# Kernel optimization log

Hardware: AMD Instinct MI355X
Metric: run time of the kernel (lower is better)

The kernel has to match this reference:

```python
import jax, jax.numpy as jnp
import numpy as np

N, E, D = 20000, 320000, 128


def _glorot(key, shape):
    fan_in, fan_out = shape[0], shape[-1]
    lim = jnp.sqrt(6.0 / (fan_in + fan_out)).astype(jnp.float32)
    return jax.random.uniform(key, shape, jnp.float32, -lim, lim)


def setup_inputs() -> dict:
    key = jax.random.key(0)
    ks = jax.random.split(key, 16)
    h = jax.random.normal(ks[0], (N, 1, D), jnp.float32)
    x = jax.random.normal(ks[1], (N, 3), jnp.float32)
    edge_index = jax.random.randint(ks[2], (2, E), 0, N, jnp.int64)
    # edge_mlp: SPDMLP(2D -> D -> D), 2 linear layers with ReLU between
    W1e = _glorot(ks[3], (2 * D, D)); b1e = jnp.zeros((D,), jnp.float32)
    W2e = _glorot(ks[4], (D, D));     b2e = jnp.zeros((D,), jnp.float32)
    # edge_inf: Linear(D, 1) + Sigmoid
    Wg = _glorot(ks[5], (D, 1));      bg = jnp.zeros((1,), jnp.float32)
    # node_mlp: SPDMLP(2D -> D -> D)
    W1n = _glorot(ks[6], (2 * D, D)); b1n = jnp.zeros((D,), jnp.float32)
    W2n = _glorot(ks[7], (D, D));     b2n = jnp.zeros((D,), jnp.float32)
    return {"h": h, "x": x, "edge_index": edge_index,
            "W1e": W1e, "b1e": b1e, "W2e": W2e, "b2e": b2e,
            "Wg": Wg, "bg": bg,
            "W1n": W1n, "b1n": b1n, "W2n": W2n, "b2n": b2n}


def _feature_joint(a, b):
    # a: [B, Na, Da], b: [B, Nb, Db] -> [B, Na+Nb, Da+Db] block-diagonal concat
    Da, Db = a.shape[2], b.shape[2]
    a_exp = jnp.concatenate([a, jnp.zeros(a.shape[:2] + (Db,), a.dtype)], axis=2)
    b_exp = jnp.concatenate([jnp.zeros(b.shape[:2] + (Da,), b.dtype), b], axis=2)
    return jnp.concatenate([a_exp, b_exp], axis=1)


def _mlp2(y, W1, b1, W2, b2):
    return jax.nn.relu(y @ W1 + b1) @ W2 + b2


def reference(h, x, edge_index, W1e, b1e, W2e, b2e, Wg, bg, W1n, b1n, W2n, b2n):
    src, dst = edge_index[0], edge_index[1]
    hi, hj = h[dst], h[src]                              # [E, 1, D] each
    mij = _mlp2(_feature_joint(hi, hj), W1e, b1e, W2e, b2e)  # [E, 2, D]
    eij = jax.nn.sigmoid(mij @ Wg + bg)                  # [E, 2, 1]
    mi = jax.ops.segment_sum(mij * eij, dst, num_segments=h.shape[0])  # [N, 2, D]
    h_new = h + _mlp2(_feature_joint(mi, h), W1n, b1n, W2n, b2n)       # [N, 3, D]
    return (h_new, x)
```

## Files before the change

### kernel.cpp

```cpp
#include <hip/hip_runtime.h>

#define D   128
#define SP  136
#define FS  132
#define NC  2
#define CAP 64

typedef __attribute__((ext_vector_type(8))) short bf16x8;
typedef __attribute__((ext_vector_type(4))) float f32x4;
typedef unsigned short u16;

__device__ __forceinline__ float sigmoidf(float v) { return 1.0f / (1.0f + __expf(-v)); }

__device__ __forceinline__ u16 f2bf(float x) {
    union { float f; unsigned u; } c; c.f = x;
    return (u16)((c.u + 0x7fffu + ((c.u >> 16) & 1u)) >> 16);
}
__device__ __forceinline__ float bflo(unsigned u) {
    union { unsigned v; float f; } c; c.v = u << 16; return c.f;
}
__device__ __forceinline__ float bfhi(unsigned u) {
    union { unsigned v; float f; } c; c.v = u & 0xffff0000u; return c.f;
}

__device__ __forceinline__ void layer_mfma(
    const u16* __restrict__ a_hi,
    const short* __restrict__ WbM, int lane, int ctbase, f32x4 acc[NC][2])
{
    #pragma unroll
    for (int ks = 0; ks < 4; ++ks) {
        bf16x8 ah[2];
        #pragma unroll
        for (int rt = 0; rt < 2; ++rt) {
            const int o = (rt * 16 + (lane & 15)) * SP + ks * 32 + (lane >> 4) * 8;
            ah[rt] = *reinterpret_cast<const bf16x8*>(a_hi + o);
        }
        #pragma unroll
        for (int c = 0; c < NC; ++c) {
            const bf16x8 bh = *reinterpret_cast<const bf16x8*>(
                WbM + ((ctbase + c) * 4 + ks) * 512 + lane * 8);
            #pragma unroll
            for (int rt = 0; rt < 2; ++rt)
                acc[c][rt] = __builtin_amdgcn_mfma_f32_16x16x32_bf16(ah[rt], bh, acc[c][rt], 0, 0, 0);
        }
    }
}

__device__ __forceinline__ void store_relu(
    const f32x4 acc[NC][2], const float b1v[NC],
    u16* __restrict__ t_hi, int lane, int ctbase)
{
    #pragma unroll
    for (int c = 0; c < NC; ++c)
        #pragma unroll
        for (int rt = 0; rt < 2; ++rt)
            #pragma unroll
            for (int rr = 0; rr < 4; ++rr) {
                const int row = rt * 16 + (lane >> 4) * 4 + rr;
                const int j   = (ctbase + c) * 16 + (lane & 15);
                t_hi[row * SP + j] = f2bf(fmaxf(acc[c][rt][rr] + b1v[c], 0.f));
            }
}

__device__ __forceinline__ void acc8(float* a, uint4 q) {
    a[0] += bflo(q.x); a[1] += bfhi(q.x);
    a[2] += bflo(q.y); a[3] += bfhi(q.y);
    a[4] += bflo(q.z); a[5] += bfhi(q.z);
    a[6] += bflo(q.w); a[7] += bfhi(q.w);
}

__device__ __forceinline__ void mlp_core(
    int base, int r, int N,
    const float* __restrict__ h,  const float* __restrict__ R0,
    const int* __restrict__ cnt,  const int* __restrict__ bucket,
    const u16* __restrict__ Q1b,  const short* __restrict__ Wb,
    const float* __restrict__ b1n, const float* __restrict__ b2n,
    float* __restrict__ out_h, u16* __restrict__ smem)
{
    u16* a_hi = smem;
    u16* t_hi = smem + 32 * SP;

    const int tid  = threadIdx.x, lane = tid & 63, w = tid >> 6;
    const int ctbase = w * NC;
    const int nl = tid >> 3, cg = tid & 7;

    if (r == 1) {
        int node = base + nl; if (node >= N) node = N - 1;
        int deg = cnt[node]; if (deg > CAP) deg = CAP;
        const int* __restrict__ bk = bucket + (size_t)node * CAP;
        const u16* __restrict__ Qc = Q1b + cg * 16;
        float a[16] = {0.f,0.f,0.f,0.f,0.f,0.f,0.f,0.f,0.f,0.f,0.f,0.f,0.f,0.f,0.f,0.f};
        for (int i = 0; i < deg; ++i) {
            const int s = bk[i];
            const uint4 qa = *reinterpret_cast<const uint4*>(Qc + (size_t)s * D);
            const uint4 qb = *reinterpret_cast<const uint4*>(Qc + (size_t)s * D + 8);
            acc8(a, qa); acc8(a + 8, qb);
        }
        union { u16 s[16]; uint4 v[2]; } ph;
        #pragma unroll
        for (int k = 0; k < 16; ++k) ph.s[k] = f2bf(a[k]);
        *reinterpret_cast<uint4*>(&a_hi[nl * SP + cg * 16])     = ph.v[0];
        *reinterpret_cast<uint4*>(&a_hi[nl * SP + cg * 16 + 8]) = ph.v[1];
    } else {
        const float* __restrict__ src = (r == 0) ? R0 : h;
        for (int idx = tid; idx < 32 * 32; idx += 256) {
            const int row = idx >> 5, c4 = (idx & 31) << 2;
            int node = base + row; if (node >= N) node = N - 1;
            float4 v = *reinterpret_cast<const float4*>(&src[(size_t)node * D + c4]);
            if (r == 0) {
                const float cv = (float)cnt[node];
                v.x *= cv; v.y *= cv; v.z *= cv; v.w *= cv;
            }
            ushort4 hi;
            hi.x = f2bf(v.x); hi.y = f2bf(v.y); hi.z = f2bf(v.z); hi.w = f2bf(v.w);
            *reinterpret_cast<ushort4*>(&a_hi[row * SP + c4]) = hi;
        }
    }
    __syncthreads();

    float b1v[NC], b2v[NC];
    #pragma unroll
    for (int c = 0; c < NC; ++c) {
        const int j = (ctbase + c) * 16 + (lane & 15);
        b1v[c] = b1n[j]; b2v[c] = b2n[j];
    }

    f32x4 acc[NC][2];
    #pragma unroll
    for (int c = 0; c < NC; ++c)
        #pragma unroll
        for (int rt = 0; rt < 2; ++rt) acc[c][rt] = (f32x4){0.f, 0.f, 0.f, 0.f};
    layer_mfma(a_hi, Wb + (size_t)((r == 2) ? 4 : 3) * 16384, lane, ctbase, acc);
    __syncthreads();
    store_relu(acc, b1v, t_hi, lane, ctbase);
    __syncthreads();

    f32x4 o[NC][2];
    #pragma unroll
    for (int c = 0; c < NC; ++c)
        #pragma unroll
        for (int rt = 0; rt < 2; ++rt) o[c][rt] = (f32x4){0.f, 0.f, 0.f, 0.f};
    layer_mfma(t_hi, Wb + (size_t)5 * 16384, lane, ctbase, o);
    __syncthreads();

    float* fs = reinterpret_cast<float*>(smem);
    #pragma unroll
    for (int c = 0; c < NC; ++c)
        #pragma unroll
        for (int rt = 0; rt < 2; ++rt)
            #pragma unroll
            for (int rr = 0; rr < 4; ++rr) {
                const int row = rt * 16 + (lane >> 4) * 4 + rr;
                const int j   = (ctbase + c) * 16 + (lane & 15);
                fs[row * FS + j] = o[c][rt][rr] + b2v[c];
            }
    __syncthreads();

    const int node = base + nl;
    if (node < N) {
        #pragma unroll
        for (int k = 0; k < 4; ++k) {
            float4 ov = *reinterpret_cast<const float4*>(&fs[nl * FS + cg * 16 + k * 4]);
            const float4 hv = *reinterpret_cast<const float4*>(&h[(size_t)node * D + cg * 16 + k * 4]);
            ov.x += hv.x; ov.y += hv.y; ov.z += hv.z; ov.w += hv.w;
            *reinterpret_cast<float4*>(&out_h[((size_t)node * 3 + r) * D + cg * 16 + k * 4]) = ov;
        }
    }
}

__global__ __launch_bounds__(256) void zero_repack_x_kernel(
    int* __restrict__ cnt, int N, int ZB,
    const float* __restrict__ W1e, const float* __restrict__ W2e,
    const float* __restrict__ W1n, const float* __restrict__ W2n,
    short* __restrict__ Wb,
    const float* __restrict__ x, float* __restrict__ out_x)
{
    const int RB = 48;
    if (blockIdx.x < (unsigned)ZB) {
        const int i = blockIdx.x * 256 + threadIdx.x;
        if (i < N) cnt[i] = 0;
        return;
    }
    if (blockIdx.x >= (unsigned)(ZB + RB)) {
        const int i4 = ((blockIdx.x - ZB - RB) * 256 + threadIdx.x) * 4;
        const int total = N * 3;
        if (i4 + 3 < total) {
            *reinterpret_cast<float4*>(&out_x[i4]) =
                *reinterpret_cast<const float4*>(&x[i4]);
        } else {
            for (int k = i4; k < total && k < i4 + 4; ++k) out_x[k] = x[k];
        }
        return;
    }
    const int gid = (blockIdx.x - ZB) * 256 + threadIdx.x;
    if (gid >= 6 * 8 * 4 * 64) return;
    const int lane = gid & 63;
    int t = gid >> 6;
    const int ks = t & 3; t >>= 2;
    const int ct = t & 7;
    const int m  = t >> 3;
    const float* src;
    switch (m) {
        case 0: src = W1e;             break;
        case 1: src = W1e + 128 * 128; break;
        case 2: src = W2e;             break;
        case 3: src = W1n;             break;
        case 4: src = W1n + 128 * 128; break;
        default: src = W2n;            break;
    }
    const int j  = ct * 16 + (lane & 15);
    const int k0 = ks * 32 + (lane >> 4) * 8;
    bf16x8 hi;
    #pragma unroll
    for (int e = 0; e < 8; ++e) hi[e] = (short)f2bf(src[(size_t)(k0 + e) * 128 + j]);
    *reinterpret_cast<bf16x8*>(Wb + (size_t)m * 16384 + (ct * 4 + ks) * 512 + lane * 8) = hi;
}

__global__ __launch_bounds__(256, 8) void pre_r2_scatter_kernel(
    const float* __restrict__ h, const short* __restrict__ Wb,
    const float* __restrict__ b1e, const float* __restrict__ b2e,
    const float* __restrict__ Wg,  const float* __restrict__ bg,
    const float* __restrict__ b1n, const float* __restrict__ b2n,
    float* __restrict__ R0, u16* __restrict__ Q1b, float* __restrict__ out_h,
    int N, int PB, int MB,
    const int* __restrict__ ei, int E, int* __restrict__ cnt, int* __restrict__ bucket)
{
    __shared__ __align__(16) u16 smem[2 * 32 * SP];
    __shared__ float red_s[4][32];

    const unsigned bid = blockIdx.x;

    if (bid >= (unsigned)(PB + MB)) {
        const int e = (bid - PB - MB) * 256 + threadIdx.x;
        if (e < E) {
            const int s = ei[e];
            const int d = ei[E + e];
            const int slot = atomicAdd(&cnt[d], 1);
            if (slot < CAP) bucket[(size_t)d * CAP + slot] = s;
        }
        return;
    }

    if (bid >= (unsigned)PB) {
        mlp_core((bid - PB) * 32, 2, N, h, R0, cnt, bucket, Q1b, Wb,
                 b1n, b2n, out_h, smem);
        return;
    }

    u16* a_hi = smem;
    u16* t_hi = smem + 32 * SP;
    const int tid  = threadIdx.x, lane = tid & 63, w = tid >> 6;
    const int hf   = bid & 1;
    const int base = (bid >> 1) * 32;
    const int ctbase = w * NC;

    for (int idx = tid; idx < 32 * 32; idx += 256) {
        const int row = idx >> 5, c4 = (idx & 31) << 2;
        int node = base + row; if (node >= N) node = N - 1;
        const float4 v = *reinterpret_cast<const float4*>(&h[(size_t)node * D + c4]);
        ushort4 hi;
        hi.x = f2bf(v.x); hi.y = f2bf(v.y); hi.z = f2bf(v.z); hi.w = f2bf(v.w);
        *reinterpret_cast<ushort4*>(&a_hi[row * SP + c4]) = hi;
    }
    __syncthreads();

    float b1v[NC], b2v[NC], wgv[NC];
    #pragma unroll
    for (int c = 0; c < NC; ++c) {
        const int j = (ctbase + c) * 16 + (lane & 15);
        b1v[c] = b1e[j]; b2v[c] = b2e[j]; wgv[c] = Wg[j];
    }
    const float bgv = bg[0];

    f32x4 acc[NC][2];
    #pragma unroll
    for (int c = 0; c < NC; ++c)
        #pragma unroll
        for (int rt = 0; rt < 2; ++rt) acc[c][rt] = (f32x4){0.f, 0.f, 0.f, 0.f};
    layer_mfma(a_hi, Wb + (size_t)hf * 16384, lane, ctbase, acc);
    __syncthreads();
    store_relu(acc, b1v, t_hi, lane, ctbase);
    __syncthreads();

    f32x4 p[NC][2];
    #pragma unroll
    for (int c = 0; c < NC; ++c)
        #pragma unroll
        for (int rt = 0; rt < 2; ++rt) p[c][rt] = (f32x4){0.f, 0.f, 0.f, 0.f};
    layer_mfma(t_hi, Wb + (size_t)2 * 16384, lane, ctbase, p);

    #pragma unroll
    for (int rt = 0; rt < 2; ++rt)
        #pragma unroll
        for (int rr = 0; rr < 4; ++rr) {
            float part = 0.f;
            #pragma unroll
            for (int c = 0; c < NC; ++c) part += (p[c][rt][rr] + b2v[c]) * wgv[c];
            #pragma unroll
            for (int m = 1; m <= 8; m <<= 1) part += __shfl_xor(part, m, 64);
            if ((lane & 15) == 0)
                red_s[w][rt * 16 + (lane >> 4) * 4 + rr] = part;
        }
    __syncthreads();

    float* fs = reinterpret_cast<float*>(smem);
    #pragma unroll
    for (int rt = 0; rt < 2; ++rt)
        #pragma unroll
        for (int rr = 0; rr < 4; ++rr) {
            const int row = rt * 16 + (lane >> 4) * 4 + rr;
            const float g = sigmoidf(red_s[0][row] + red_s[1][row] +
                                     red_s[2][row] + red_s[3][row] + bgv);
            #pragma unroll
            for (int c = 0; c < NC; ++c) {
                const int j = (ctbase + c) * 16 + (lane & 15);
                fs[row * FS + j] = (p[c][rt][rr] + b2v[c]) * g;
            }
        }
    __syncthreads();

    const int nl = tid >> 3, cg = tid & 7;
    const int node = base + nl;
    if (node < N) {
        if (hf == 0) {
            #pragma unroll
            for (int k = 0; k < 4; ++k) {
                const float4 v = *reinterpret_cast<const float4*>(&fs[nl * FS + cg * 16 + k * 4]);
                *reinterpret_cast<float4*>(&R0[(size_t)node * D + cg * 16 + k * 4]) = v;
            }
        } else {
            union { u16 s[16]; uint4 v[2]; } pk;
            #pragma unroll
            for (int k = 0; k < 16; ++k) pk.s[k] = f2bf(fs[nl * FS + cg * 16 + k]);
            *reinterpret_cast<uint4*>(&Q1b[(size_t)node * D + cg * 16])     = pk.v[0];
            *reinterpret_cast<uint4*>(&Q1b[(size_t)node * D + cg * 16 + 8]) = pk.v[1];
        }
    }
}

__global__ __launch_bounds__(256, 8) void mlp_r01_kernel(
    const float* __restrict__ h,  const float* __restrict__ R0,
    const int* __restrict__ cnt,  const int* __restrict__ bucket,
    const u16* __restrict__ Q1b,  const short* __restrict__ Wb,
    const float* __restrict__ b1n, const float* __restrict__ b2n,
    float* __restrict__ out_h, int N, int RT1)
{
    __shared__ __align__(16) u16 smem[2 * 32 * SP];

    int r, tile;
    if (blockIdx.x < (unsigned)RT1) { r = 1; tile = blockIdx.x; }
    else                            { r = 0; tile = blockIdx.x - RT1; }

    mlp_core(tile * 32, r, N, h, R0, cnt, bucket, Q1b, Wb,
             b1n, b2n, out_h, smem);
}

extern "C" void kernel_launch(void* const* d_in, const int* in_sizes, int n_in,
                              void* d_out, int out_size, void* d_ws, size_t ws_size,
                              hipStream_t stream)
{
    const float* h   = (const float*)d_in[0];
    const float* x   = (const float*)d_in[1];
    const int*   ei  = (const int*)d_in[2];
    const float* W1e = (const float*)d_in[3];
    const float* b1e = (const float*)d_in[4];
    const float* W2e = (const float*)d_in[5];
    const float* b2e = (const float*)d_in[6];
    const float* Wg  = (const float*)d_in[7];
    const float* bg  = (const float*)d_in[8];
    const float* W1n = (const float*)d_in[9];
    const float* b1n = (const float*)d_in[10];
    const float* W2n = (const float*)d_in[11];
    const float* b2n = (const float*)d_in[12];

    const int N = in_sizes[0] / D;
    const int E = in_sizes[2] / 2;

    float* R0     = (float*)d_ws;
    u16*   Q1b    = (u16*)(R0 + (size_t)N * D);
    short* Wb     = (short*)(Q1b + (size_t)N * D);
    int*   cnt    = (int*)(Wb + 6 * 16384);
    int*   bucket = cnt + N;

    float* out_h = (float*)d_out;
    float* out_x = out_h + (size_t)N * 3 * D;

    const int ntiles = (N + 31) / 32;
    const int ZB = (N + 255) / 256;
    const int RB = 48;
    const int XB = (N * 3 + 1023) / 1024;
    const int PB = ntiles * 2;
    const int MB = ntiles;
    const int SB = (E + 255) / 256;

    zero_repack_x_kernel<<<ZB + RB + XB, 256, 0, stream>>>(cnt, N, ZB,
                                                           W1e, W2e, W1n, W2n, Wb, x, out_x);
    pre_r2_scatter_kernel<<<PB + MB + SB, 256, 0, stream>>>(h, Wb, b1e, b2e, Wg, bg,
                                                            b1n, b2n, R0, Q1b, out_h,
                                                            N, PB, MB, ei, E, cnt, bucket);
    mlp_r01_kernel<<<ntiles * 2, 256, 0, stream>>>(h, R0, cnt, bucket, Q1b, Wb,
                                                   b1n, b2n, out_h, N, ntiles);
}
```

Before: 67.22 us.

## Give each wave its own 16-row tile to remove block-level barriers

Restructures the MLP kernels so each wavefront owns an independent 16-node tile with a private LDS plane and computes all 8 output column tiles itself. This removes the __syncthreads between layers and the cross-wave reduction for the gate. The scatter blocks are moved to the front of the grid, and the gather loop is unrolled by two with wider per-lane chunks. In exchange, each wave uses more registers (launch bounds drop to 5 blocks), and every wave must read the full weight matrix, which raises weight read traffic.

```diff
diff --git a/kernel.cpp b/kernel.cpp
--- a/kernel.cpp
+++ b/kernel.cpp
@@ -2,8 +2,6 @@
 
 #define D   128
 #define SP  136
-#define FS  132
-#define NC  2
 #define CAP 64
 
 typedef __attribute__((ext_vector_type(8))) short bf16x8;
@@ -22,46 +20,6 @@
 __device__ __forceinline__ float bfhi(unsigned u) {
     union { unsigned v; float f; } c; c.v = u & 0xffff0000u; return c.f;
 }
-
-__device__ __forceinline__ void layer_mfma(
-    const u16* __restrict__ a_hi,
-    const short* __restrict__ WbM, int lane, int ctbase, f32x4 acc[NC][2])
-{
-    #pragma unroll
-    for (int ks = 0; ks < 4; ++ks) {
-        bf16x8 ah[2];
-        #pragma unroll
-        for (int rt = 0; rt < 2; ++rt) {
-            const int o = (rt * 16 + (lane & 15)) * SP + ks * 32 + (lane >> 4) * 8;
-            ah[rt] = *reinterpret_cast<const bf16x8*>(a_hi + o);
-        }
-        #pragma unroll
-        for (int c = 0; c < NC; ++c) {
-            const bf16x8 bh = *reinterpret_cast<const bf16x8*>(
-                WbM + ((ctbase + c) * 4 + ks) * 512 + lane * 8);
-            #pragma unroll
-            for (int rt = 0; rt < 2; ++rt)
-                acc[c][rt] = __builtin_amdgcn_mfma_f32_16x16x32_bf16(ah[rt], bh, acc[c][rt], 0, 0, 0);
-        }
-    }
-}
-
-__device__ __forceinline__ void store_relu(
-    const f32x4 acc[NC][2], const float b1v[NC],
-    u16* __restrict__ t_hi, int lane, int ctbase)
-{
-    #pragma unroll
-    for (int c = 0; c < NC; ++c)
-        #pragma unroll
-        for (int rt = 0; rt < 2; ++rt)
-            #pragma unroll
-            for (int rr = 0; rr < 4; ++rr) {
-                const int row = rt * 16 + (lane >> 4) * 4 + rr;
-                const int j   = (ctbase + c) * 16 + (lane & 15);
-                t_hi[row * SP + j] = f2bf(fmaxf(acc[c][rt][rr] + b1v[c], 0.f));
-            }
-}
-
 __device__ __forceinline__ void acc8(float* a, uint4 q) {
     a[0] += bflo(q.x); a[1] += bfhi(q.x);
     a[2] += bflo(q.y); a[3] += bfhi(q.y);
@@ -69,101 +27,106 @@
     a[6] += bflo(q.w); a[7] += bfhi(q.w);
 }
 
-__device__ __forceinline__ void mlp_core(
-    int base, int r, int N,
-    const float* __restrict__ h,  const float* __restrict__ R0,
-    const int* __restrict__ cnt,  const int* __restrict__ bucket,
-    const u16* __restrict__ Q1b,  const short* __restrict__ Wb,
-    const float* __restrict__ b1n, const float* __restrict__ b2n,
-    float* __restrict__ out_h, u16* __restrict__ smem)
-{
-    u16* a_hi = smem;
-    u16* t_hi = smem + 32 * SP;
-
-    const int tid  = threadIdx.x, lane = tid & 63, w = tid >> 6;
-    const int ctbase = w * NC;
-    const int nl = tid >> 3, cg = tid & 7;
-
-    if (r == 1) {
-        int node = base + nl; if (node >= N) node = N - 1;
-        int deg = cnt[node]; if (deg > CAP) deg = CAP;
-        const int* __restrict__ bk = bucket + (size_t)node * CAP;
-        const u16* __restrict__ Qc = Q1b + cg * 16;
-        float a[16] = {0.f,0.f,0.f,0.f,0.f,0.f,0.f,0.f,0.f,0.f,0.f,0.f,0.f,0.f,0.f,0.f};
-        for (int i = 0; i < deg; ++i) {
-            const int s = bk[i];
-            const uint4 qa = *reinterpret_cast<const uint4*>(Qc + (size_t)s * D);
-            const uint4 qb = *reinterpret_cast<const uint4*>(Qc + (size_t)s * D + 8);
-            acc8(a, qa); acc8(a + 8, qb);
-        }
-        union { u16 s[16]; uint4 v[2]; } ph;
-        #pragma unroll
-        for (int k = 0; k < 16; ++k) ph.s[k] = f2bf(a[k]);
-        *reinterpret_cast<uint4*>(&a_hi[nl * SP + cg * 16])     = ph.v[0];
-        *reinterpret_cast<uint4*>(&a_hi[nl * SP + cg * 16 + 8]) = ph.v[1];
-    } else {
-        const float* __restrict__ src = (r == 0) ? R0 : h;
-        for (int idx = tid; idx < 32 * 32; idx += 256) {
-            const int row = idx >> 5, c4 = (idx & 31) << 2;
-            int node = base + row; if (node >= N) node = N - 1;
-            float4 v = *reinterpret_cast<const float4*>(&src[(size_t)node * D + c4]);
-            if (r == 0) {
-                const float cv = (float)cnt[node];
-                v.x *= cv; v.y *= cv; v.z *= cv; v.w *= cv;
+__device__ __forceinline__ void layer16(const u16* __restrict__ plane,
+                                        const short* __restrict__ WbM,
+                                        int lane, f32x4 acc[8])
+{
+    #pragma unroll
+    for (int ks = 0; ks < 4; ++ks) {
+        const bf16x8 a = *reinterpret_cast<const bf16x8*>(
+            plane + (lane & 15) * SP + ks * 32 + (lane >> 4) * 8);
+        #pragma unroll
+        for (int ct = 0; ct < 8; ++ct) {
+            const bf16x8 b = *reinterpret_cast<const bf16x8*>(
+                WbM + (ct * 4 + ks) * 512 + lane * 8);
+            acc[ct] = __builtin_amdgcn_mfma_f32_16x16x32_bf16(a, b, acc[ct], 0, 0, 0);
+        }
+    }
+}
+
+__device__ __forceinline__ void store_t(const f32x4 acc[8], const float b1v[8],
+                                        u16* __restrict__ plane, int lane)
+{
+    #pragma unroll
+    for (int ct = 0; ct < 8; ++ct)
+        #pragma unroll
+        for (int rr = 0; rr < 4; ++rr)
+            plane[((lane >> 4) * 4 + rr) * SP + ct * 16 + (lane & 15)] =
+                f2bf(fmaxf(acc[ct][rr] + b1v[ct], 0.f));
+}
+
+__device__ __forceinline__ void stage16(const float* __restrict__ src,
+                                        const int* __restrict__ cnt,
+                                        int base, int N, int lane,
+                                        u16* __restrict__ plane)
+{
+    #pragma unroll
+    for (int it = 0; it < 8; ++it) {
+        const int idx = it * 64 + lane;
+        const int row = idx >> 5, c4 = (idx & 31) << 2;
+        int node = base + row; if (node >= N) node = N - 1;
+        float4 v = *reinterpret_cast<const float4*>(&src[(size_t)node * D + c4]);
+        if (cnt) { const float cv = (float)cnt[node]; v.x *= cv; v.y *= cv; v.z *= cv; v.w *= cv; }
+        ushort4 s; s.x = f2bf(v.x); s.y = f2bf(v.y); s.z = f2bf(v.z); s.w = f2bf(v.w);
+        *reinterpret_cast<ushort4*>(&plane[row * SP + c4]) = s;
+    }
+}
+
+__device__ __forceinline__ void epi_f32(const f32x4 o[8], const float b2v[8],
+                                        const float* g, const float* __restrict__ hres,
+                                        float* __restrict__ dst, int drs,
+                                        int base, int N, int lane,
+                                        u16* __restrict__ plane)
+{
+    float* pf = reinterpret_cast<float*>(plane);
+    #pragma unroll
+    for (int ph = 0; ph < 2; ++ph) {
+        const int grp = lane >> 4;
+        if ((grp >> 1) == ph) {
+            const int lr4 = (grp & 1) * 4;
+            #pragma unroll
+            for (int ct = 0; ct < 8; ++ct)
+                #pragma unroll
+                for (int rr = 0; rr < 4; ++rr) {
+                    float v = o[ct][rr] + b2v[ct];
+                    if (g) v *= g[rr];
+                    pf[(lr4 + rr) * 132 + ct * 16 + (lane & 15)] = v;
+                }
+        }
+        const int row  = ph * 8 + (lane >> 3);
+        const int node = base + row;
+        const int c16  = (lane & 7) * 16;
+        if (node < N) {
+            #pragma unroll
+            for (int k = 0; k < 4; ++k) {
+                float4 v = *reinterpret_cast<const float4*>(&pf[(lane >> 3) * 132 + c16 + k * 4]);
+                if (hres) {
+                    const float4 hv = *reinterpret_cast<const float4*>(&hres[(size_t)node * D + c16 + k * 4]);
+                    v.x += hv.x; v.y += hv.y; v.z += hv.z; v.w += hv.w;
+                }
+                *reinterpret_cast<float4*>(&dst[(size_t)node * drs + c16 + k * 4]) = v;
             }
-            ushort4 hi;
-            hi.x = f2bf(v.x); hi.y = f2bf(v.y); hi.z = f2bf(v.z); hi.w = f2bf(v.w);
-            *reinterpret_cast<ushort4*>(&a_hi[row * SP + c4]) = hi;
-        }
-    }
-    __syncthreads();
-
-    float b1v[NC], b2v[NC];
-    #pragma unroll
-    for (int c = 0; c < NC; ++c) {
-        const int j = (ctbase + c) * 16 + (lane & 15);
-        b1v[c] = b1n[j]; b2v[c] = b2n[j];
-    }
-
-    f32x4 acc[NC][2];
-    #pragma unroll
-    for (int c = 0; c < NC; ++c)
-        #pragma unroll
-        for (int rt = 0; rt < 2; ++rt) acc[c][rt] = (f32x4){0.f, 0.f, 0.f, 0.f};
-    layer_mfma(a_hi, Wb + (size_t)((r == 2) ? 4 : 3) * 16384, lane, ctbase, acc);
-    __syncthreads();
-    store_relu(acc, b1v, t_hi, lane, ctbase);
-    __syncthreads();
-
-    f32x4 o[NC][2];
-    #pragma unroll
-    for (int c = 0; c < NC; ++c)
-        #pragma unroll
-        for (int rt = 0; rt < 2; ++rt) o[c][rt] = (f32x4){0.f, 0.f, 0.f, 0.f};
-    layer_mfma(t_hi, Wb + (size_t)5 * 16384, lane, ctbase, o);
-    __syncthreads();
-
-    float* fs = reinterpret_cast<float*>(smem);
-    #pragma unroll
-    for (int c = 0; c < NC; ++c)
-        #pragma unroll
-        for (int rt = 0; rt < 2; ++rt)
-            #pragma unroll
-            for (int rr = 0; rr < 4; ++rr) {
-                const int row = rt * 16 + (lane >> 4) * 4 + rr;
-                const int j   = (ctbase + c) * 16 + (lane & 15);
-                fs[row * FS + j] = o[c][rt][rr] + b2v[c];
-            }
-    __syncthreads();
-
-    const int node = base + nl;
+        }
+    }
+}
+
+__device__ __forceinline__ void epi_q1b(const f32x4 p[8], const float b2v[8], const float g[4],
+                                        u16* __restrict__ Q1b, int base, int N, int lane,
+                                        u16* __restrict__ plane)
+{
+    #pragma unroll
+    for (int ct = 0; ct < 8; ++ct)
+        #pragma unroll
+        for (int rr = 0; rr < 4; ++rr)
+            plane[((lane >> 4) * 4 + rr) * SP + ct * 16 + (lane & 15)] =
+                f2bf((p[ct][rr] + b2v[ct]) * g[rr]);
+    const int row = lane >> 2, c32 = (lane & 3) * 32;
+    const int node = base + row;
     if (node < N) {
         #pragma unroll
         for (int k = 0; k < 4; ++k) {
-            float4 ov = *reinterpret_cast<const float4*>(&fs[nl * FS + cg * 16 + k * 4]);
-            const float4 hv = *reinterpret_cast<const float4*>(&h[(size_t)node * D + cg * 16 + k * 4]);
-            ov.x += hv.x; ov.y += hv.y; ov.z += hv.z; ov.w += hv.w;
-            *reinterpret_cast<float4*>(&out_h[((size_t)node * 3 + r) * D + cg * 16 + k * 4]) = ov;
+            const uint4 v = *reinterpret_cast<const uint4*>(&plane[row * SP + c32 + k * 8]);
+            *reinterpret_cast<uint4*>(&Q1b[(size_t)node * D + c32 + k * 8]) = v;
         }
     }
 }
@@ -216,22 +179,22 @@
     *reinterpret_cast<bf16x8*>(Wb + (size_t)m * 16384 + (ct * 4 + ks) * 512 + lane * 8) = hi;
 }
 
-__global__ __launch_bounds__(256, 8) void pre_r2_scatter_kernel(
+__global__ __launch_bounds__(256, 5) void k2_scatter_pre_r2(
     const float* __restrict__ h, const short* __restrict__ Wb,
     const float* __restrict__ b1e, const float* __restrict__ b2e,
     const float* __restrict__ Wg,  const float* __restrict__ bg,
     const float* __restrict__ b1n, const float* __restrict__ b2n,
     float* __restrict__ R0, u16* __restrict__ Q1b, float* __restrict__ out_h,
-    int N, int PB, int MB,
+    int N, int SB, int PT,
     const int* __restrict__ ei, int E, int* __restrict__ cnt, int* __restrict__ bucket)
 {
-    __shared__ __align__(16) u16 smem[2 * 32 * SP];
-    __shared__ float red_s[4][32];
-
+    __shared__ __align__(16) u16 smem[4 * 16 * SP];
+    const int tid = threadIdx.x, lane = tid & 63, w = tid >> 6;
+    u16* plane = smem + w * 16 * SP;
     const unsigned bid = blockIdx.x;
 
-    if (bid >= (unsigned)(PB + MB)) {
-        const int e = (bid - PB - MB) * 256 + threadIdx.x;
+    if (bid < (unsigned)SB) {
+        const int e = bid * 256 + tid;
         if (e < E) {
             const int s = ei[e];
             const int d = ei[E + e];
@@ -240,119 +203,144 @@
         }
         return;
     }
-
-    if (bid >= (unsigned)PB) {
-        mlp_core((bid - PB) * 32, 2, N, h, R0, cnt, bucket, Q1b, Wb,
-                 b1n, b2n, out_h, smem);
-        return;
-    }
-
-    u16* a_hi = smem;
-    u16* t_hi = smem + 32 * SP;
-    const int tid  = threadIdx.x, lane = tid & 63, w = tid >> 6;
-    const int hf   = bid & 1;
-    const int base = (bid >> 1) * 32;
-    const int ctbase = w * NC;
-
-    for (int idx = tid; idx < 32 * 32; idx += 256) {
-        const int row = idx >> 5, c4 = (idx & 31) << 2;
-        int node = base + row; if (node >= N) node = N - 1;
-        const float4 v = *reinterpret_cast<const float4*>(&h[(size_t)node * D + c4]);
-        ushort4 hi;
-        hi.x = f2bf(v.x); hi.y = f2bf(v.y); hi.z = f2bf(v.z); hi.w = f2bf(v.w);
-        *reinterpret_cast<ushort4*>(&a_hi[row * SP + c4]) = hi;
-    }
-    __syncthreads();
-
-    float b1v[NC], b2v[NC], wgv[NC];
-    #pragma unroll
-    for (int c = 0; c < NC; ++c) {
-        const int j = (ctbase + c) * 16 + (lane & 15);
-        b1v[c] = b1e[j]; b2v[c] = b2e[j]; wgv[c] = Wg[j];
-    }
-    const float bgv = bg[0];
-
-    f32x4 acc[NC][2];
-    #pragma unroll
-    for (int c = 0; c < NC; ++c)
-        #pragma unroll
-        for (int rt = 0; rt < 2; ++rt) acc[c][rt] = (f32x4){0.f, 0.f, 0.f, 0.f};
-    layer_mfma(a_hi, Wb + (size_t)hf * 16384, lane, ctbase, acc);
-    __syncthreads();
-    store_relu(acc, b1v, t_hi, lane, ctbase);
-    __syncthreads();
-
-    f32x4 p[NC][2];
-    #pragma unroll
-    for (int c = 0; c < NC; ++c)
-        #pragma unroll
-        for (int rt = 0; rt < 2; ++rt) p[c][rt] = (f32x4){0.f, 0.f, 0.f, 0.f};
-    layer_mfma(t_hi, Wb + (size_t)2 * 16384, lane, ctbase, p);
-
-    #pragma unroll
-    for (int rt = 0; rt < 2; ++rt)
+    const int t = bid - SB;
+
+    if (t < PT) {
+        const int hf   = t & 1;
+        const int base = (t >> 1) * 64 + w * 16;
+        stage16(h, nullptr, base, N, lane, plane);
+
+        float b1v[8], b2v[8], wgv[8];
+        #pragma unroll
+        for (int ct = 0; ct < 8; ++ct) {
+            const int j = ct * 16 + (lane & 15);
+            b1v[ct] = b1e[j]; b2v[ct] = b2e[j]; wgv[ct] = Wg[j];
+        }
+        const float bgv = bg[0];
+
+        f32x4 acc[8];
+        #pragma unroll
+        for (int ct = 0; ct < 8; ++ct) acc[ct] = (f32x4){0.f, 0.f, 0.f, 0.f};
+        layer16(plane, Wb + (size_t)hf * 16384, lane, acc);
+        store_t(acc, b1v, plane, lane);
+
+        f32x4 p[8];
+        #pragma unroll
+        for (int ct = 0; ct < 8; ++ct) p[ct] = (f32x4){0.f, 0.f, 0.f, 0.f};
+        layer16(plane, Wb + (size_t)2 * 16384, lane, p);
+
+        float g[4];
         #pragma unroll
         for (int rr = 0; rr < 4; ++rr) {
             float part = 0.f;
             #pragma unroll
-            for (int c = 0; c < NC; ++c) part += (p[c][rt][rr] + b2v[c]) * wgv[c];
+            for (int ct = 0; ct < 8; ++ct) part += (p[ct][rr] + b2v[ct]) * wgv[ct];
             #pragma unroll
             for (int m = 1; m <= 8; m <<= 1) part += __shfl_xor(part, m, 64);
-            if ((lane & 15) == 0)
-                red_s[w][rt * 16 + (lane >> 4) * 4 + rr] = part;
-        }
-    __syncthreads();
-
-    float* fs = reinterpret_cast<float*>(smem);
-    #pragma unroll
-    for (int rt = 0; rt < 2; ++rt)
-        #pragma unroll
-        for (int rr = 0; rr < 4; ++rr) {
-            const int row = rt * 16 + (lane >> 4) * 4 + rr;
-            const float g = sigmoidf(red_s[0][row] + red_s[1][row] +
-                                     red_s[2][row] + red_s[3][row] + bgv);
-            #pragma unroll
-            for (int c = 0; c < NC; ++c) {
-                const int j = (ctbase + c) * 16 + (lane & 15);
-                fs[row * FS + j] = (p[c][rt][rr] + b2v[c]) * g;
-            }
-        }
-    __syncthreads();
-
-    const int nl = tid >> 3, cg = tid & 7;
-    const int node = base + nl;
-    if (node < N) {
-        if (hf == 0) {
-            #pragma unroll
-            for (int k = 0; k < 4; ++k) {
-                const float4 v = *reinterpret_cast<const float4*>(&fs[nl * FS + cg * 16 + k * 4]);
-                *reinterpret_cast<float4*>(&R0[(size_t)node * D + cg * 16 + k * 4]) = v;
-            }
-        } else {
-            union { u16 s[16]; uint4 v[2]; } pk;
-            #pragma unroll
-            for (int k = 0; k < 16; ++k) pk.s[k] = f2bf(fs[nl * FS + cg * 16 + k]);
-            *reinterpret_cast<uint4*>(&Q1b[(size_t)node * D + cg * 16])     = pk.v[0];
-            *reinterpret_cast<uint4*>(&Q1b[(size_t)node * D + cg * 16 + 8]) = pk.v[1];
-        }
-    }
-}
-
-__global__ __launch_bounds__(256, 8) void mlp_r01_kernel(
+            g[rr] = sigmoidf(part + bgv);
+        }
+
+        if (hf == 0) epi_f32(p, b2v, g, nullptr, R0, D, base, N, lane, plane);
+        else         epi_q1b(p, b2v, g, Q1b, base, N, lane, plane);
+        return;
+    }
+
+    const int base = (t - PT) * 64 + w * 16;
+    stage16(h, nullptr, base, N, lane, plane);
+
+    float b1v[8], b2v[8];
+    #pragma unroll
+    for (int ct = 0; ct < 8; ++ct) {
+        const int j = ct * 16 + (lane & 15);
+        b1v[ct] = b1n[j]; b2v[ct] = b2n[j];
+    }
+
+    f32x4 acc[8];
+    #pragma unroll
+    for (int ct = 0; ct < 8; ++ct) acc[ct] = (f32x4){0.f, 0.f, 0.f, 0.f};
+    layer16(plane, Wb + (size_t)4 * 16384, lane, acc);
+    store_t(acc, b1v, plane, lane);
+
+    f32x4 o[8];
+    #pragma unroll
+    for (int ct = 0; ct < 8; ++ct) o[ct] = (f32x4){0.f, 0.f, 0.f, 0.f};
+    layer16(plane, Wb + (size_t)5 * 16384, lane, o);
+
+    epi_f32(o, b2v, nullptr, h, out_h + 2 * D, 3 * D, base, N, lane, plane);
+}
+
+__global__ __launch_bounds__(256, 5) void k3_r1_r0(
     const float* __restrict__ h,  const float* __restrict__ R0,
     const int* __restrict__ cnt,  const int* __restrict__ bucket,
     const u16* __restrict__ Q1b,  const short* __restrict__ Wb,
     const float* __restrict__ b1n, const float* __restrict__ b2n,
-    float* __restrict__ out_h, int N, int RT1)
-{
-    __shared__ __align__(16) u16 smem[2 * 32 * SP];
+    float* __restrict__ out_h, int N, int RT)
+{
+    __shared__ __align__(16) u16 smem[4 * 16 * SP];
+    const int tid = threadIdx.x, lane = tid & 63, w = tid >> 6;
+    u16* plane = smem + w * 16 * SP;
 
     int r, tile;
-    if (blockIdx.x < (unsigned)RT1) { r = 1; tile = blockIdx.x; }
-    else                            { r = 0; tile = blockIdx.x - RT1; }
-
-    mlp_core(tile * 32, r, N, h, R0, cnt, bucket, Q1b, Wb,
-             b1n, b2n, out_h, smem);
+    if (blockIdx.x < (unsigned)RT) { r = 1; tile = blockIdx.x; }
+    else                           { r = 0; tile = blockIdx.x - RT; }
+    const int base = tile * 64 + w * 16;
+
+    if (r == 1) {
+        const int nloc = lane >> 2, c32 = (lane & 3) * 32;
+        int node = base + nloc; if (node >= N) node = N - 1;
+        int deg = cnt[node]; if (deg > CAP) deg = CAP;
+        const int* __restrict__ bk = bucket + (size_t)node * CAP;
+        float a[32];
+        #pragma unroll
+        for (int k = 0; k < 32; ++k) a[k] = 0.f;
+        int i = 0;
+        for (; i + 1 < deg; i += 2) {
+            const int s0 = bk[i], s1 = bk[i + 1];
+            const u16* q0 = Q1b + (size_t)s0 * D + c32;
+            const u16* q1 = Q1b + (size_t)s1 * D + c32;
+            #pragma unroll
+            for (int k = 0; k < 4; ++k) {
+                acc8(&a[k * 8], *reinterpret_cast<const uint4*>(q0 + k * 8));
+                acc8(&a[k * 8], *reinterpret_cast<const uint4*>(q1 + k * 8));
+            }
+        }
+        if (i < deg) {
+            const int s = bk[i];
+            const u16* q = Q1b + (size_t)s * D + c32;
+            #pragma unroll
+            for (int k = 0; k < 4; ++k)
+                acc8(&a[k * 8], *reinterpret_cast<const uint4*>(q + k * 8));
+        }
+        #pragma unroll
+        for (int k4 = 0; k4 < 8; ++k4) {
+            ushort4 s4;
+            s4.x = f2bf(a[k4 * 4 + 0]); s4.y = f2bf(a[k4 * 4 + 1]);
+            s4.z = f2bf(a[k4 * 4 + 2]); s4.w = f2bf(a[k4 * 4 + 3]);
+            *reinterpret_cast<ushort4*>(&plane[nloc * SP + c32 + k4 * 4]) = s4;
+        }
+    } else {
+        stage16(R0, cnt, base, N, lane, plane);
+    }
+
+    float b1v[8], b2v[8];
+    #pragma unroll
+    for (int ct = 0; ct < 8; ++ct) {
+        const int j = ct * 16 + (lane & 15);
+        b1v[ct] = b1n[j]; b2v[ct] = b2n[j];
+    }
+
+    f32x4 acc[8];
+    #pragma unroll
+    for (int ct = 0; ct < 8; ++ct) acc[ct] = (f32x4){0.f, 0.f, 0.f, 0.f};
+    layer16(plane, Wb + (size_t)3 * 16384, lane, acc);
+    store_t(acc, b1v, plane, lane);
+
+    f32x4 o[8];
+    #pragma unroll
+    for (int ct = 0; ct < 8; ++ct) o[ct] = (f32x4){0.f, 0.f, 0.f, 0.f};
+    layer16(plane, Wb + (size_t)5 * 16384, lane, o);
+
+    epi_f32(o, b2v, nullptr, h, out_h + r * D, 3 * D, base, N, lane, plane);
 }
 
 extern "C" void kernel_launch(void* const* d_in, const int* in_sizes, int n_in,
@@ -385,19 +373,18 @@
     float* out_h = (float*)d_out;
     float* out_x = out_h + (size_t)N * 3 * D;
 
-    const int ntiles = (N + 31) / 32;
+    const int nt64 = (N + 63) / 64;
     const int ZB = (N + 255) / 256;
     const int RB = 48;
     const int XB = (N * 3 + 1023) / 1024;
-    const int PB = ntiles * 2;
-    const int MB = ntiles;
     const int SB = (E + 255) / 256;
+    const int PT = nt64 * 2;
 
     zero_repack_x_kernel<<<ZB + RB + XB, 256, 0, stream>>>(cnt, N, ZB,
                                                            W1e, W2e, W1n, W2n, Wb, x, out_x);
-    pre_r2_scatter_kernel<<<PB + MB + SB, 256, 0, stream>>>(h, Wb, b1e, b2e, Wg, bg,
-                                                            b1n, b2n, R0, Q1b, out_h,
-                                                            N, PB, MB, ei, E, cnt, bucket);
-    mlp_r01_kernel<<<ntiles * 2, 256, 0, stream>>>(h, R0, cnt, bucket, Q1b, Wb,
-                                                   b1n, b2n, out_h, N, ntiles);
-}
+    k2_scatter_pre_r2<<<SB + PT + nt64, 256, 0, stream>>>(h, Wb, b1e, b2e, Wg, bg,
+                                                          b1n, b2n, R0, Q1b, out_h,
+                                                          N, SB, PT, ei, E, cnt, bucket);
+    k3_r1_r0<<<nt64 * 2, 256, 0, stream>>>(h, R0, cnt, bucket, Q1b, Wb,
+                                           b1n, b2n, out_h, N, nt64);
+}
```

Measured after the change: 91.47 us. +36.1%, slower.

## Use 64-node tiles with register-preloaded weights in fused MLP kernels

Applied to the files above, without the earlier changes.

Doubles the node tile from 32 to 64 rows, so each wave issues four row-tiles of MFMAs per weight fragment. Both layers' weight fragments are preloaded into registers before staging, and one barrier between layers is dropped. The gather loop is widened and unrolled by two, and the bf16 output path writes through shared memory to get vectorized stores. The cost is higher register and LDS use (launch bounds lowered to 3 blocks) and half as many blocks, so occupancy drops.

```diff
diff --git a/kernel.cpp b/kernel.cpp
--- a/kernel.cpp
+++ b/kernel.cpp
@@ -1,10 +1,12 @@
 #include <hip/hip_runtime.h>
 
-#define D   128
-#define SP  136
-#define FS  132
-#define NC  2
-#define CAP 64
+#define D    128
+#define SP   136
+#define FS   132
+#define NC   2
+#define NR   4
+#define TN   64
+#define CAP  64
 
 typedef __attribute__((ext_vector_type(8))) short bf16x8;
 typedef __attribute__((ext_vector_type(4))) float f32x4;
@@ -22,46 +24,6 @@
 __device__ __forceinline__ float bfhi(unsigned u) {
     union { unsigned v; float f; } c; c.v = u & 0xffff0000u; return c.f;
 }
-
-__device__ __forceinline__ void layer_mfma(
-    const u16* __restrict__ a_hi,
-    const short* __restrict__ WbM, int lane, int ctbase, f32x4 acc[NC][2])
-{
-    #pragma unroll
-    for (int ks = 0; ks < 4; ++ks) {
-        bf16x8 ah[2];
-        #pragma unroll
-        for (int rt = 0; rt < 2; ++rt) {
-            const int o = (rt * 16 + (lane & 15)) * SP + ks * 32 + (lane >> 4) * 8;
-            ah[rt] = *reinterpret_cast<const bf16x8*>(a_hi + o);
-        }
-        #pragma unroll
-        for (int c = 0; c < NC; ++c) {
-            const bf16x8 bh = *reinterpret_cast<const bf16x8*>(
-                WbM + ((ctbase + c) * 4 + ks) * 512 + lane * 8);
-            #pragma unroll
-            for (int rt = 0; rt < 2; ++rt)
-                acc[c][rt] = __builtin_amdgcn_mfma_f32_16x16x32_bf16(ah[rt], bh, acc[c][rt], 0, 0, 0);
-        }
-    }
-}
-
-__device__ __forceinline__ void store_relu(
-    const f32x4 acc[NC][2], const float b1v[NC],
-    u16* __restrict__ t_hi, int lane, int ctbase)
-{
-    #pragma unroll
-    for (int c = 0; c < NC; ++c)
-        #pragma unroll
-        for (int rt = 0; rt < 2; ++rt)
-            #pragma unroll
-            for (int rr = 0; rr < 4; ++rr) {
-                const int row = rt * 16 + (lane >> 4) * 4 + rr;
-                const int j   = (ctbase + c) * 16 + (lane & 15);
-                t_hi[row * SP + j] = f2bf(fmaxf(acc[c][rt][rr] + b1v[c], 0.f));
-            }
-}
-
 __device__ __forceinline__ void acc8(float* a, uint4 q) {
     a[0] += bflo(q.x); a[1] += bfhi(q.x);
     a[2] += bflo(q.y); a[3] += bfhi(q.y);
@@ -69,7 +31,69 @@
     a[6] += bflo(q.w); a[7] += bfhi(q.w);
 }
 
-__device__ __forceinline__ void mlp_core(
+__device__ __forceinline__ void preload_w(const short* __restrict__ WbM,
+                                          int lane, int ctbase, bf16x8 w[4 * NC])
+{
+    #pragma unroll
+    for (int ks = 0; ks < 4; ++ks)
+        #pragma unroll
+        for (int c = 0; c < NC; ++c)
+            w[ks * NC + c] = *reinterpret_cast<const bf16x8*>(
+                WbM + ((ctbase + c) * 4 + ks) * 512 + lane * 8);
+}
+
+__device__ __forceinline__ void layer64(
+    const u16* __restrict__ plane, const bf16x8 w[4 * NC],
+    int lane, f32x4 acc[NC][NR])
+{
+    #pragma unroll
+    for (int ks = 0; ks < 4; ++ks) {
+        bf16x8 a[NR];
+        #pragma unroll
+        for (int rt = 0; rt < NR; ++rt)
+            a[rt] = *reinterpret_cast<const bf16x8*>(
+                plane + (rt * 16 + (lane & 15)) * SP + ks * 32 + (lane >> 4) * 8);
+        #pragma unroll
+        for (int c = 0; c < NC; ++c) {
+            const bf16x8 b = w[ks * NC + c];
+            #pragma unroll
+            for (int rt = 0; rt < NR; ++rt)
+                acc[c][rt] = __builtin_amdgcn_mfma_f32_16x16x32_bf16(a[rt], b, acc[c][rt], 0, 0, 0);
+        }
+    }
+}
+
+__device__ __forceinline__ void store_t(
+    const f32x4 acc[NC][NR], const float b1v[NC],
+    u16* __restrict__ dst, int lane, int ctbase)
+{
+    #pragma unroll
+    for (int c = 0; c < NC; ++c)
+        #pragma unroll
+        for (int rt = 0; rt < NR; ++rt)
+            #pragma unroll
+            for (int rr = 0; rr < 4; ++rr)
+                dst[(rt * 16 + (lane >> 4) * 4 + rr) * SP + (ctbase + c) * 16 + (lane & 15)] =
+                    f2bf(fmaxf(acc[c][rt][rr] + b1v[c], 0.f));
+}
+
+__device__ __forceinline__ void stage64(
+    const float* __restrict__ src, const int* __restrict__ cnt,
+    int base, int N, int tid, u16* __restrict__ plane)
+{
+    #pragma unroll
+    for (int it = 0; it < 8; ++it) {
+        const int idx = it * 256 + tid;
+        const int row = idx >> 5, c4 = (idx & 31) << 2;
+        int node = base + row; if (node >= N) node = N - 1;
+        float4 v = *reinterpret_cast<const float4*>(&src[(size_t)node * D + c4]);
+        if (cnt) { const float cv = (float)cnt[node]; v.x *= cv; v.y *= cv; v.z *= cv; v.w *= cv; }
+        ushort4 s; s.x = f2bf(v.x); s.y = f2bf(v.y); s.z = f2bf(v.z); s.w = f2bf(v.w);
+        *reinterpret_cast<ushort4*>(&plane[row * SP + c4]) = s;
+    }
+}
+
+__device__ __forceinline__ void mlp_core64(
     int base, int r, int N,
     const float* __restrict__ h,  const float* __restrict__ R0,
     const int* __restrict__ cnt,  const int* __restrict__ bucket,
@@ -77,44 +101,51 @@
     const float* __restrict__ b1n, const float* __restrict__ b2n,
     float* __restrict__ out_h, u16* __restrict__ smem)
 {
-    u16* a_hi = smem;
-    u16* t_hi = smem + 32 * SP;
-
-    const int tid  = threadIdx.x, lane = tid & 63, w = tid >> 6;
+    u16* P1 = smem;
+    u16* P2 = smem + TN * SP;
+    const int tid = threadIdx.x, lane = tid & 63, w = tid >> 6;
     const int ctbase = w * NC;
-    const int nl = tid >> 3, cg = tid & 7;
+
+    bf16x8 wA[4 * NC], wB[4 * NC];
+    preload_w(Wb + (size_t)((r == 2) ? 4 : 3) * 16384, lane, ctbase, wA);
+    preload_w(Wb + (size_t)5 * 16384, lane, ctbase, wB);
 
     if (r == 1) {
+        const int nl = tid >> 2, c32 = (tid & 3) * 32;
         int node = base + nl; if (node >= N) node = N - 1;
         int deg = cnt[node]; if (deg > CAP) deg = CAP;
         const int* __restrict__ bk = bucket + (size_t)node * CAP;
-        const u16* __restrict__ Qc = Q1b + cg * 16;
-        float a[16] = {0.f,0.f,0.f,0.f,0.f,0.f,0.f,0.f,0.f,0.f,0.f,0.f,0.f,0.f,0.f,0.f};
-        for (int i = 0; i < deg; ++i) {
+        const u16* __restrict__ Qc = Q1b + c32;
+        float a[32];
+        #pragma unroll
+        for (int k = 0; k < 32; ++k) a[k] = 0.f;
+        int i = 0;
+        for (; i + 1 < deg; i += 2) {
+            const int s0 = bk[i], s1 = bk[i + 1];
+            const u16* q0 = Qc + (size_t)s0 * D;
+            const u16* q1 = Qc + (size_t)s1 * D;
+            #pragma unroll
+            for (int k = 0; k < 4; ++k) {
+                acc8(&a[k * 8], *reinterpret_cast<const uint4*>(q0 + k * 8));
+                acc8(&a[k * 8], *reinterpret_cast<const uint4*>(q1 + k * 8));
+            }
+        }
+        if (i < deg) {
             const int s = bk[i];
-            const uint4 qa = *reinterpret_cast<const uint4*>(Qc + (size_t)s * D);
-            const uint4 qb = *reinterpret_cast<const uint4*>(Qc + (size_t)s * D + 8);
-            acc8(a, qa); acc8(a + 8, qb);
-        }
-        union { u16 s[16]; uint4 v[2]; } ph;
-        #pragma unroll
-        for (int k = 0; k < 16; ++k) ph.s[k] = f2bf(a[k]);
-        *reinterpret_cast<uint4*>(&a_hi[nl * SP + cg * 16])     = ph.v[0];
-        *reinterpret_cast<uint4*>(&a_hi[nl * SP + cg * 16 + 8]) = ph.v[1];
+            const u16* q = Qc + (size_t)s * D;
+            #pragma unroll
+            for (int k = 0; k < 4; ++k)
+                acc8(&a[k * 8], *reinterpret_cast<const uint4*>(q + k * 8));
+        }
+        #pragma unroll
+        for (int k4 = 0; k4 < 8; ++k4) {
+            ushort4 s4;
+            s4.x = f2bf(a[k4 * 4 + 0]); s4.y = f2bf(a[k4 * 4 + 1]);
+            s4.z = f2bf(a[k4 * 4 + 2]); s4.w = f2bf(a[k4 * 4 + 3]);
+            *reinterpret_cast<ushort4*>(&P1[nl * SP + c32 + k4 * 4]) = s4;
+        }
     } else {
-        const float* __restrict__ src = (r == 0) ? R0 : h;
-        for (int idx = tid; idx < 32 * 32; idx += 256) {
-            const int row = idx >> 5, c4 = (idx & 31) << 2;
-            int node = base + row; if (node >= N) node = N - 1;
-            float4 v = *reinterpret_cast<const float4*>(&src[(size_t)node * D + c4]);
-            if (r == 0) {
-                const float cv = (float)cnt[node];
-                v.x *= cv; v.y *= cv; v.z *= cv; v.w *= cv;
-            }
-            ushort4 hi;
-            hi.x = f2bf(v.x); hi.y = f2bf(v.y); hi.z = f2bf(v.z); hi.w = f2bf(v.w);
-            *reinterpret_cast<ushort4*>(&a_hi[row * SP + c4]) = hi;
-        }
+        stage64((r == 0) ? R0 : h, (r == 0) ? cnt : nullptr, base, N, tid, P1);
     }
     __syncthreads();
 
@@ -125,45 +156,43 @@
         b1v[c] = b1n[j]; b2v[c] = b2n[j];
     }
 
-    f32x4 acc[NC][2];
-    #pragma unroll
-    for (int c = 0; c < NC; ++c)
-        #pragma unroll
-        for (int rt = 0; rt < 2; ++rt) acc[c][rt] = (f32x4){0.f, 0.f, 0.f, 0.f};
-    layer_mfma(a_hi, Wb + (size_t)((r == 2) ? 4 : 3) * 16384, lane, ctbase, acc);
-    __syncthreads();
-    store_relu(acc, b1v, t_hi, lane, ctbase);
-    __syncthreads();
-
-    f32x4 o[NC][2];
-    #pragma unroll
-    for (int c = 0; c < NC; ++c)
-        #pragma unroll
-        for (int rt = 0; rt < 2; ++rt) o[c][rt] = (f32x4){0.f, 0.f, 0.f, 0.f};
-    layer_mfma(t_hi, Wb + (size_t)5 * 16384, lane, ctbase, o);
+    f32x4 acc[NC][NR];
+    #pragma unroll
+    for (int c = 0; c < NC; ++c)
+        #pragma unroll
+        for (int rt = 0; rt < NR; ++rt) acc[c][rt] = (f32x4){0.f, 0.f, 0.f, 0.f};
+    layer64(P1, wA, lane, acc);
+    store_t(acc, b1v, P2, lane, ctbase);
+    __syncthreads();
+
+    f32x4 o[NC][NR];
+    #pragma unroll
+    for (int c = 0; c < NC; ++c)
+        #pragma unroll
+        for (int rt = 0; rt < NR; ++rt) o[c][rt] = (f32x4){0.f, 0.f, 0.f, 0.f};
+    layer64(P2, wB, lane, o);
     __syncthreads();
 
     float* fs = reinterpret_cast<float*>(smem);
     #pragma unroll
     for (int c = 0; c < NC; ++c)
         #pragma unroll
-        for (int rt = 0; rt < 2; ++rt)
-            #pragma unroll
-            for (int rr = 0; rr < 4; ++rr) {
-                const int row = rt * 16 + (lane >> 4) * 4 + rr;
-                const int j   = (ctbase + c) * 16 + (lane & 15);
-                fs[row * FS + j] = o[c][rt][rr] + b2v[c];
-            }
-    __syncthreads();
-
+        for (int rt = 0; rt < NR; ++rt)
+            #pragma unroll
+            for (int rr = 0; rr < 4; ++rr)
+                fs[(rt * 16 + (lane >> 4) * 4 + rr) * FS + (ctbase + c) * 16 + (lane & 15)] =
+                    o[c][rt][rr] + b2v[c];
+    __syncthreads();
+
+    const int nl = tid >> 2, cg = tid & 3;
     const int node = base + nl;
     if (node < N) {
         #pragma unroll
-        for (int k = 0; k < 4; ++k) {
-            float4 ov = *reinterpret_cast<const float4*>(&fs[nl * FS + cg * 16 + k * 4]);
-            const float4 hv = *reinterpret_cast<const float4*>(&h[(size_t)node * D + cg * 16 + k * 4]);
+        for (int k = 0; k < 8; ++k) {
+            float4 ov = *reinterpret_cast<const float4*>(&fs[nl * FS + cg * 32 + k * 4]);
+            const float4 hv = *reinterpret_cast<const float4*>(&h[(size_t)node * D + cg * 32 + k * 4]);
             ov.x += hv.x; ov.y += hv.y; ov.z += hv.z; ov.w += hv.w;
-            *reinterpret_cast<float4*>(&out_h[((size_t)node * 3 + r) * D + cg * 16 + k * 4]) = ov;
+            *reinterpret_cast<float4*>(&out_h[((size_t)node * 3 + r) * D + cg * 32 + k * 4]) = ov;
         }
     }
 }
@@ -216,7 +245,7 @@
     *reinterpret_cast<bf16x8*>(Wb + (size_t)m * 16384 + (ct * 4 + ks) * 512 + lane * 8) = hi;
 }
 
-__global__ __launch_bounds__(256, 8) void pre_r2_scatter_kernel(
+__global__ __launch_bounds__(256, 3) void pre_r2_scatter_kernel(
     const float* __restrict__ h, const short* __restrict__ Wb,
     const float* __restrict__ b1e, const float* __restrict__ b2e,
     const float* __restrict__ Wg,  const float* __restrict__ bg,
@@ -225,8 +254,10 @@
     int N, int PB, int MB,
     const int* __restrict__ ei, int E, int* __restrict__ cnt, int* __restrict__ bucket)
 {
-    __shared__ __align__(16) u16 smem[2 * 32 * SP];
-    __shared__ float red_s[4][32];
+    __shared__ __align__(16) u16 smem[2 * TN * SP];
+    __shared__ float red_s[4][TN];
+    u16* P1 = smem;
+    u16* P2 = smem + TN * SP;
 
     const unsigned bid = blockIdx.x;
 
@@ -242,26 +273,21 @@
     }
 
     if (bid >= (unsigned)PB) {
-        mlp_core((bid - PB) * 32, 2, N, h, R0, cnt, bucket, Q1b, Wb,
-                 b1n, b2n, out_h, smem);
+        mlp_core64((bid - PB) * TN, 2, N, h, nullptr, nullptr, nullptr, Q1b, Wb,
+                   b1n, b2n, out_h, smem);
         return;
     }
 
-    u16* a_hi = smem;
-    u16* t_hi = smem + 32 * SP;
-    const int tid  = threadIdx.x, lane = tid & 63, w = tid >> 6;
+    const int tid = threadIdx.x, lane = tid & 63, w = tid >> 6;
     const int hf   = bid & 1;
-    const int base = (bid >> 1) * 32;
+    const int base = (bid >> 1) * TN;
     const int ctbase = w * NC;
 
-    for (int idx = tid; idx < 32 * 32; idx += 256) {
-        const int row = idx >> 5, c4 = (idx & 31) << 2;
-        int node = base + row; if (node >= N) node = N - 1;
-        const float4 v = *reinterpret_cast<const float4*>(&h[(size_t)node * D + c4]);
-        ushort4 hi;
-        hi.x = f2bf(v.x); hi.y = f2bf(v.y); hi.z = f2bf(v.z); hi.w = f2bf(v.w);
-        *reinterpret_cast<ushort4*>(&a_hi[row * SP + c4]) = hi;
-    }
+    bf16x8 wA[4 * NC], wB[4 * NC];
+    preload_w(Wb + (size_t)hf * 16384, lane, ctbase, wA);
+    preload_w(Wb + (size_t)2  * 16384, lane, ctbase, wB);
+
+    stage64(h, nullptr, base, N, tid, P1);
     __syncthreads();
 
     float b1v[NC], b2v[NC], wgv[NC];
@@ -272,25 +298,24 @@
     }
     const float bgv = bg[0];
 
-    f32x4 acc[NC][2];
-    #pragma unroll
-    for (int c = 0; c < NC; ++c)
-        #pragma unroll
-        for (int rt = 0; rt < 2; ++rt) acc[c][rt] = (f32x4){0.f, 0.f, 0.f, 0.f};
-    layer_mfma(a_hi, Wb + (size_t)hf * 16384, lane, ctbase, acc);
-    __syncthreads();
-    store_relu(acc, b1v, t_hi, lane, ctbase);
-    __syncthreads();
-
-    f32x4 p[NC][2];
-    #pragma unroll
-    for (int c = 0; c < NC; ++c)
-        #pragma unroll
-        for (int rt = 0; rt < 2; ++rt) p[c][rt] = (f32x4){0.f, 0.f, 0.f, 0.f};
-    layer_mfma(t_hi, Wb + (size_t)2 * 16384, lane, ctbase, p);
-
-    #pragma unroll
-    for (int rt = 0; rt < 2; ++rt)
+    f32x4 acc[NC][NR];
+    #pragma unroll
+    for (int c = 0; c < NC; ++c)
+        #pragma unroll
+        for (int rt = 0; rt < NR; ++rt) acc[c][rt] = (f32x4){0.f, 0.f, 0.f, 0.f};
+    layer64(P1, wA, lane, acc);
+    store_t(acc, b1v, P2, lane, ctbase);
+    __syncthreads();
+
+    f32x4 p[NC][NR];
+    #pragma unroll
+    for (int c = 0; c < NC; ++c)
+        #pragma unroll
+        for (int rt = 0; rt < NR; ++rt) p[c][rt] = (f32x4){0.f, 0.f, 0.f, 0.f};
+    layer64(P2, wB, lane, p);
+
+    #pragma unroll
+    for (int rt = 0; rt < NR; ++rt)
         #pragma unroll
         for (int rr = 0; rr < 4; ++rr) {
             float part = 0.f;
@@ -303,56 +328,73 @@
         }
     __syncthreads();
 
-    float* fs = reinterpret_cast<float*>(smem);
-    #pragma unroll
-    for (int rt = 0; rt < 2; ++rt)
+    float g[NR][4];
+    #pragma unroll
+    for (int rt = 0; rt < NR; ++rt)
         #pragma unroll
         for (int rr = 0; rr < 4; ++rr) {
             const int row = rt * 16 + (lane >> 4) * 4 + rr;
-            const float g = sigmoidf(red_s[0][row] + red_s[1][row] +
-                                     red_s[2][row] + red_s[3][row] + bgv);
-            #pragma unroll
-            for (int c = 0; c < NC; ++c) {
-                const int j = (ctbase + c) * 16 + (lane & 15);
-                fs[row * FS + j] = (p[c][rt][rr] + b2v[c]) * g;
+            g[rt][rr] = sigmoidf(red_s[0][row] + red_s[1][row] +
+                                 red_s[2][row] + red_s[3][row] + bgv);
+        }
+
+    if (hf == 0) {
+        float* fs = reinterpret_cast<float*>(smem);
+        #pragma unroll
+        for (int c = 0; c < NC; ++c)
+            #pragma unroll
+            for (int rt = 0; rt < NR; ++rt)
+                #pragma unroll
+                for (int rr = 0; rr < 4; ++rr)
+                    fs[(rt * 16 + (lane >> 4) * 4 + rr) * FS + (ctbase + c) * 16 + (lane & 15)] =
+                        (p[c][rt][rr] + b2v[c]) * g[rt][rr];
+        __syncthreads();
+        const int nl = tid >> 2, cg = tid & 3;
+        const int node = base + nl;
+        if (node < N) {
+            #pragma unroll
+            for (int k = 0; k < 8; ++k) {
+                const float4 v = *reinterpret_cast<const float4*>(&fs[nl * FS + cg * 32 + k * 4]);
+                *reinterpret_cast<float4*>(&R0[(size_t)node * D + cg * 32 + k * 4]) = v;
             }
         }
-    __syncthreads();
-
-    const int nl = tid >> 3, cg = tid & 7;
-    const int node = base + nl;
-    if (node < N) {
-        if (hf == 0) {
+    } else {
+        #pragma unroll
+        for (int c = 0; c < NC; ++c)
+            #pragma unroll
+            for (int rt = 0; rt < NR; ++rt)
+                #pragma unroll
+                for (int rr = 0; rr < 4; ++rr)
+                    P1[(rt * 16 + (lane >> 4) * 4 + rr) * SP + (ctbase + c) * 16 + (lane & 15)] =
+                        f2bf((p[c][rt][rr] + b2v[c]) * g[rt][rr]);
+        __syncthreads();
+        const int nl = tid >> 2, cg = tid & 3;
+        const int node = base + nl;
+        if (node < N) {
             #pragma unroll
             for (int k = 0; k < 4; ++k) {
-                const float4 v = *reinterpret_cast<const float4*>(&fs[nl * FS + cg * 16 + k * 4]);
-                *reinterpret_cast<float4*>(&R0[(size_t)node * D + cg * 16 + k * 4]) = v;
+                const uint4 v = *reinterpret_cast<const uint4*>(&P1[nl * SP + cg * 32 + k * 8]);
+                *reinterpret_cast<uint4*>(&Q1b[(size_t)node * D + cg * 32 + k * 8]) = v;
             }
-        } else {
-            union { u16 s[16]; uint4 v[2]; } pk;
-            #pragma unroll
-            for (int k = 0; k < 16; ++k) pk.s[k] = f2bf(fs[nl * FS + cg * 16 + k]);
-            *reinterpret_cast<uint4*>(&Q1b[(size_t)node * D + cg * 16])     = pk.v[0];
-            *reinterpret_cast<uint4*>(&Q1b[(size_t)node * D + cg * 16 + 8]) = pk.v[1];
-        }
-    }
-}
-
-__global__ __launch_bounds__(256, 8) void mlp_r01_kernel(
+        }
+    }
+}
+
+__global__ __launch_bounds__(256, 3) void mlp_r01_kernel(
     const float* __restrict__ h,  const float* __restrict__ R0,
     const int* __restrict__ cnt,  const int* __restrict__ bucket,
     const u16* __restrict__ Q1b,  const short* __restrict__ Wb,
     const float* __restrict__ b1n, const float* __restrict__ b2n,
     float* __restrict__ out_h, int N, int RT1)
 {
-    __shared__ __align__(16) u16 smem[2 * 32 * SP];
+    __shared__ __align__(16) u16 smem[2 * TN * SP];
 
     int r, tile;
     if (blockIdx.x < (unsigned)RT1) { r = 1; tile = blockIdx.x; }
     else                            { r = 0; tile = blockIdx.x - RT1; }
 
-    mlp_core(tile * 32, r, N, h, R0, cnt, bucket, Q1b, Wb,
-             b1n, b2n, out_h, smem);
+    mlp_core64(tile * TN, r, N, h, R0, cnt, bucket, Q1b, Wb,
+               b1n, b2n, out_h, smem);
 }
 
 extern "C" void kernel_launch(void* const* d_in, const int* in_sizes, int n_in,
@@ -385,12 +427,12 @@
     float* out_h = (float*)d_out;
     float* out_x = out_h + (size_t)N * 3 * D;
 
-    const int ntiles = (N + 31) / 32;
+    const int nt64 = (N + TN - 1) / TN;
     const int ZB = (N + 255) / 256;
     const int RB = 48;
     const int XB = (N * 3 + 1023) / 1024;
-    const int PB = ntiles * 2;
-    const int MB = ntiles;
+    const int PB = nt64 * 2;
+    const int MB = nt64;
     const int SB = (E + 255) / 256;
 
     zero_repack_x_kernel<<<ZB + RB + XB, 256, 0, stream>>>(cnt, N, ZB,
@@ -398,6 +440,6 @@
     pre_r2_scatter_kernel<<<PB + MB + SB, 256, 0, stream>>>(h, Wb, b1e, b2e, Wg, bg,
                                                             b1n, b2n, R0, Q1b, out_h,
                                                             N, PB, MB, ei, E, cnt, bucket);
-    mlp_r01_kernel<<<ntiles * 2, 256, 0, stream>>>(h, R0, cnt, bucket, Q1b, Wb,
-                                                   b1n, b2n, out_h, N, ntiles);
-}
+    mlp_r01_kernel<<<nt64 * 2, 256, 0, stream>>>(h, R0, cnt, bucket, Q1b, Wb,
+                                                 b1n, b2n, out_h, N, nt64);
+}
```

New measurement: 75.03 us. 11.6% more time.
